# Performance work log

Measured on AMD Instinct MI355X. Metric: run time of the kernel, lower is better.

## Reference

```python
import jax, jax.numpy as jnp
import numpy as np

VOXEL_DIM = (64, 64, 64)
VOXEL_SIZE = 0.04
STRIDE = 4.0  # backbone2d_stride


def setup_inputs() -> dict:
    key = jax.random.key(0)
    k1, k2 = jax.random.split(key, 2)
    bs, nv, cin, h, w = 4, 12, 384, 64, 64
    cout = 32
    vit_feats = jax.random.normal(k1, (bs, nv, cin, h, w), dtype=jnp.float32)
    w_reduce = jax.random.normal(k2, (cout, cin), dtype=jnp.float32) * 0.05
    b_reduce = jnp.zeros((cout,), dtype=jnp.float32)
    # Realistic pinhole projections: K @ [I | t], camera ~3m from grid center.
    rng = np.random.default_rng(0)
    f, cx, cy = 128.0, 128.0, 128.0
    K = np.array([[f, 0.0, cx], [0.0, f, cy], [0.0, 0.0, 1.0]])
    projs = np.zeros((bs, nv, 3, 4), dtype=np.float32)
    for v in range(nv):
        t = np.array([0.2 * rng.standard_normal(), 0.2 * rng.standard_normal(),
                      3.0 + 0.3 * rng.standard_normal()])
        E = np.concatenate([np.eye(3), t[:, None]], axis=1)  # 3x4
        projs[:, v] = (K @ E).astype(np.float32)
    return {"vit_feats": vit_feats, "w_reduce": w_reduce,
            "b_reduce": b_reduce, "projection": jnp.asarray(projs)}


def _backproject(proj, feats):
    """proj: (b,3,4), feats: (b,c,h,w) -> volume (b,c,N), valid (b,N)."""
    nx, ny, nz = VOXEL_DIM
    N = nx * ny * nz
    b, c, h, w = feats.shape
    X, Y, Z = jnp.meshgrid(jnp.arange(nx), jnp.arange(ny), jnp.arange(nz), indexing='ij')
    coords = jnp.stack([X.ravel(), Y.ravel(), Z.ravel()]).astype(feats.dtype)  # (3, N)
    origin = jnp.array([[-nx * VOXEL_SIZE / 2],
                        [-ny * VOXEL_SIZE / 2],
                        [-nz * VOXEL_SIZE / 2]], dtype=feats.dtype)
    world = coords * VOXEL_SIZE + origin                    # (3, N)
    world = jnp.concatenate([world, jnp.ones((1, N), feats.dtype)], axis=0)  # (4, N)
    cam = jnp.einsum('bij,jn->bin', proj, world)            # (b, 3, N)
    px = jnp.round(cam[:, 0] / cam[:, 2]).astype(jnp.int32)
    py = jnp.round(cam[:, 1] / cam[:, 2]).astype(jnp.int32)
    pz = cam[:, 2]
    valid = (px >= 0) & (py >= 0) & (px < w) & (py < h) & (pz > 0)  # (b, N)
    pxc = jnp.clip(px, 0, w - 1)
    pyc = jnp.clip(py, 0, h - 1)
    # per-batch gather: feats[b, :, py, px]
    gath = jax.vmap(lambda f, yy, xx: f[:, yy, xx])(feats, pyc, pxc)  # (b, c, N)
    vol = jnp.where(valid[:, None, :], gath, jnp.zeros((), feats.dtype))
    return vol, valid


def reference(vit_feats, w_reduce, b_reduce, projection):
    bs, nv, cin, h, w = vit_feats.shape
    cout = w_reduce.shape[0]
    nx, ny, nz = VOXEL_DIM
    N = nx * ny * nz
    # 1x1 conv channel reduction
    feats = jnp.einsum('bnchw,oc->bnohw', vit_feats, w_reduce) \
            + b_reduce[None, None, :, None, None]
    # divide intrinsics rows by the 2D backbone stride
    proj = projection.at[:, :, :2, :].set(projection[:, :, :2, :] / STRIDE)
    feats_v = jnp.moveaxis(feats, 1, 0)   # (nv, b, c, h, w)
    proj_v = jnp.moveaxis(proj, 1, 0)     # (nv, b, 3, 4)

    def step(carry, xs):
        vol, cnt = carry
        p, f = xs
        v, m = _backproject(p, f)
        return (vol + v, cnt + m.astype(vol.dtype)), None

    vol0 = jnp.zeros((bs, cout, N), jnp.float32)
    cnt0 = jnp.zeros((bs, N), jnp.float32)
    (vol, cnt), _ = jax.lax.scan(step, (vol0, cnt0), (proj_v, feats_v))
    # volume / valid, zeroed where never observed
    cnt_b = cnt[:, None, :]
    out = jnp.where(cnt_b > 0, vol / jnp.maximum(cnt_b, 1.0), jnp.zeros((), vol.dtype))
    return out.reshape(bs, cout, nx, ny, nz)
```

## Files before the change

kernel.cpp:

```cpp
#include <hip/hip_runtime.h>

#define NV 12
#define CIN 384
#define COUT 32
#define HW 4096
#define NVOX 262144
#define KSTEPS 12
#define KSTEP 32
#define KPAD 33
#define PIXB 128
#define ZROW_U4 786432

typedef __attribute__((ext_vector_type(8))) short short8v;
typedef __attribute__((ext_vector_type(4))) short short4v;
typedef __attribute__((ext_vector_type(4))) float f32x4;

__device__ __forceinline__ short bf16b(float x) {
    union { float f; unsigned u; } c; c.f = x;
    unsigned r = (c.u + 0x7fffu + ((c.u >> 16) & 1u)) >> 16;
    return (short)r;
}

__global__ __launch_bounds__(256) void w_prep_kernel(
    const float* __restrict__ w, short* __restrict__ wfrag,
    short* __restrict__ feats)
{
    const int t = blockIdx.x * 256 + threadIdx.x;
    if (t < 48 * 32) {
        const int sg = t >> 5, o = t & 31;
        const int s = sg >> 2, g = sg & 3;
        short8v v;
#pragma unroll
        for (int i = 0; i < 8; ++i)
            v[i] = bf16b(w[o * CIN + s * 32 + g * 8 + i]);
        *reinterpret_cast<short8v*>(wfrag + t * 8) = v;
    } else if (t >= 1536 && t < 1540) {
        reinterpret_cast<uint4*>(feats)[ZROW_U4 + (t - 1536)] =
            make_uint4(0u, 0u, 0u, 0u);
    }
}

__global__ __launch_bounds__(256) void mv_reduce_mfma_kernel(
    const float* __restrict__ vit, const short* __restrict__ wfrag,
    const float* __restrict__ bias, short* __restrict__ feats)
{
    __shared__ float lds[PIXB][KPAD];

    const int bid  = blockIdx.x;
    const int bv   = bid >> 5;
    const int pix0 = (bid & 31) * PIXB;

    const int tid  = threadIdx.x;
    const int wave = tid >> 6;
    const int l    = tid & 63;
    const int col  = l & 15;
    const int g    = l >> 4;

    const int kk  = tid >> 4;
    const int px4 = (tid & 15) * 4;

    const float* vbase = vit + (size_t)bv * CIN * HW + pix0;
    const short8v* wf  = reinterpret_cast<const short8v*>(wfrag);

    f32x4 acc00 = {0.f, 0.f, 0.f, 0.f};
    f32x4 acc01 = {0.f, 0.f, 0.f, 0.f};
    f32x4 acc10 = {0.f, 0.f, 0.f, 0.f};
    f32x4 acc11 = {0.f, 0.f, 0.f, 0.f};

#pragma unroll
    for (int s = 0; s < KSTEPS; ++s) {
        const float* r0base = vbase + (size_t)(s * KSTEP + kk) * HW;
        const float* r1base = vbase + (size_t)(s * KSTEP + kk + 16) * HW;
        const float4 r00 = *reinterpret_cast<const float4*>(r0base + px4);
        const float4 r01 = *reinterpret_cast<const float4*>(r0base + px4 + 64);
        const float4 r10 = *reinterpret_cast<const float4*>(r1base + px4);
        const float4 r11 = *reinterpret_cast<const float4*>(r1base + px4 + 64);

        __syncthreads();
        lds[px4 + 0][kk] = r00.x;  lds[px4 + 1][kk] = r00.y;
        lds[px4 + 2][kk] = r00.z;  lds[px4 + 3][kk] = r00.w;
        lds[px4 + 64][kk] = r01.x; lds[px4 + 65][kk] = r01.y;
        lds[px4 + 66][kk] = r01.z; lds[px4 + 67][kk] = r01.w;
        lds[px4 + 0][kk + 16] = r10.x;  lds[px4 + 1][kk + 16] = r10.y;
        lds[px4 + 2][kk + 16] = r10.z;  lds[px4 + 3][kk + 16] = r10.w;
        lds[px4 + 64][kk + 16] = r11.x; lds[px4 + 65][kk + 16] = r11.y;
        lds[px4 + 66][kk + 16] = r11.z; lds[px4 + 67][kk + 16] = r11.w;
        __syncthreads();

        const float4 f0a = *reinterpret_cast<const float4*>(&lds[wave * 32 + col][8 * g]);
        const float4 f0b = *reinterpret_cast<const float4*>(&lds[wave * 32 + col][8 * g + 4]);
        const float4 f1a = *reinterpret_cast<const float4*>(&lds[wave * 32 + 16 + col][8 * g]);
        const float4 f1b = *reinterpret_cast<const float4*>(&lds[wave * 32 + 16 + col][8 * g + 4]);

        short8v bfr0, bfr1;
        bfr0[0] = bf16b(f0a.x); bfr0[1] = bf16b(f0a.y);
        bfr0[2] = bf16b(f0a.z); bfr0[3] = bf16b(f0a.w);
        bfr0[4] = bf16b(f0b.x); bfr0[5] = bf16b(f0b.y);
        bfr0[6] = bf16b(f0b.z); bfr0[7] = bf16b(f0b.w);
        bfr1[0] = bf16b(f1a.x); bfr1[1] = bf16b(f1a.y);
        bfr1[2] = bf16b(f1a.z); bfr1[3] = bf16b(f1a.w);
        bfr1[4] = bf16b(f1b.x); bfr1[5] = bf16b(f1b.y);
        bfr1[6] = bf16b(f1b.z); bfr1[7] = bf16b(f1b.w);

        const short8v a0 = wf[(s * 4 + g) * 32 + col];
        const short8v a1 = wf[(s * 4 + g) * 32 + 16 + col];

        acc00 = __builtin_amdgcn_mfma_f32_16x16x32_bf16(a0, bfr0, acc00, 0, 0, 0);
        acc01 = __builtin_amdgcn_mfma_f32_16x16x32_bf16(a1, bfr0, acc01, 0, 0, 0);
        acc10 = __builtin_amdgcn_mfma_f32_16x16x32_bf16(a0, bfr1, acc10, 0, 0, 0);
        acc11 = __builtin_amdgcn_mfma_f32_16x16x32_bf16(a1, bfr1, acc11, 0, 0, 0);
    }

    const float4 b0 = *reinterpret_cast<const float4*>(bias + 4 * g);
    const float4 b1 = *reinterpret_cast<const float4*>(bias + 16 + 4 * g);
    short* dst0 = feats + ((size_t)bv * HW + pix0 + wave * 32 + col) * COUT;
    short* dst1 = dst0 + 16 * COUT;
    short4v o00, o01, o10, o11;
    o00[0] = bf16b(acc00[0] + b0.x); o00[1] = bf16b(acc00[1] + b0.y);
    o00[2] = bf16b(acc00[2] + b0.z); o00[3] = bf16b(acc00[3] + b0.w);
    o01[0] = bf16b(acc01[0] + b1.x); o01[1] = bf16b(acc01[1] + b1.y);
    o01[2] = bf16b(acc01[2] + b1.z); o01[3] = bf16b(acc01[3] + b1.w);
    o10[0] = bf16b(acc10[0] + b0.x); o10[1] = bf16b(acc10[1] + b0.y);
    o10[2] = bf16b(acc10[2] + b0.z); o10[3] = bf16b(acc10[3] + b0.w);
    o11[0] = bf16b(acc11[0] + b1.x); o11[1] = bf16b(acc11[1] + b1.y);
    o11[2] = bf16b(acc11[2] + b1.z); o11[3] = bf16b(acc11[3] + b1.w);
    *reinterpret_cast<short4v*>(dst0 + 4 * g) = o00;
    *reinterpret_cast<short4v*>(dst0 + 16 + 4 * g) = o01;
    *reinterpret_cast<short4v*>(dst1 + 4 * g) = o10;
    *reinterpret_cast<short4v*>(dst1 + 16 + 4 * g) = o11;
}

__global__ __launch_bounds__(256) void mv_fuse_kernel(
    const unsigned short* __restrict__ feats, const float* __restrict__ proj,
    float* __restrict__ out)
{
    __shared__ double P[NV][12];

    const int tid = threadIdx.x;
    const unsigned gid = blockIdx.x * 256u + tid;
    const unsigned vox = gid >> 2;
    const int r = tid & 3;
    const int lane = tid & 63;
    const int b = vox >> 18;
    const int n = vox & (NVOX - 1);

    if (tid < NV * 12) {
        const int v = tid / 12, e = tid - v * 12;
        const int row = e >> 2;
        const float s = (row < 2) ? 0.25f : 1.0f;
        P[v][e] = (double)(proj[((b * NV + v) * 3 + row) * 4 + (e & 3)] * s);
    }
    __syncthreads();

    const int k = n & 63, j = (n >> 6) & 63, i = n >> 12;
    const double wx = (double)i * 0.04 - 1.28;
    const double wy = (double)j * 0.04 - 1.28;
    const double wz = (double)k * 0.04 - 1.28;

    int off[3];
    int cnt = 0;
    const int bbase = b * (NV * HW * 4);
#pragma unroll
    for (int s = 0; s < 3; ++s) {
        const double* p = P[4 * s + r];
        const double cz = p[8] * wx + p[9] * wy + p[10] * wz + p[11];
        const double cx = p[0] * wx + p[1] * wy + p[2] * wz + p[3];
        const double cy = p[4] * wx + p[5] * wy + p[6] * wz + p[7];
        const double u = rint(cx / cz);
        const double t = rint(cy / cz);
        const bool valid = (cz > 0.0) & (u >= 0.0) & (u <= 63.0) &
                           (t >= 0.0) & (t <= 63.0);
        const double uc = fmin(fmax(u, 0.0), 63.0);
        const double tc = fmin(fmax(t, 0.0), 63.0);
        const int pix = (int)uc + 64 * (int)tc;
        off[s] = valid ? (bbase + ((4 * s + r) * HW + pix) * 4) : ZROW_U4;
        cnt += valid ? 1 : 0;
    }
    cnt += __shfl_xor(cnt, 1);
    cnt += __shfl_xor(cnt, 2);

    float acc[8];
#pragma unroll
    for (int q = 0; q < 8; ++q) acc[q] = 0.0f;

    const uint4* f4 = reinterpret_cast<const uint4*>(feats);
#pragma unroll
    for (int v = 0; v < NV; ++v) {
        const int src = (lane & ~3) | (v & 3);
        const int ov = __shfl(off[v >> 2], src, 64);
        const uint4 u4 = f4[ov + r];
        acc[0] += __uint_as_float(u4.x << 16);
        acc[1] += __uint_as_float(u4.x & 0xffff0000u);
        acc[2] += __uint_as_float(u4.y << 16);
        acc[3] += __uint_as_float(u4.y & 0xffff0000u);
        acc[4] += __uint_as_float(u4.z << 16);
        acc[5] += __uint_as_float(u4.z & 0xffff0000u);
        acc[6] += __uint_as_float(u4.w << 16);
        acc[7] += __uint_as_float(u4.w & 0xffff0000u);
    }

    const float sc = (cnt > 0) ? (1.0f / (float)cnt) : 0.0f;
    float* ob = out + (size_t)b * COUT * NVOX + (size_t)(8 * r) * NVOX + n;
#pragma unroll
    for (int q = 0; q < 8; ++q)
        ob[(size_t)q * NVOX] = acc[q] * sc;
}

extern "C" void kernel_launch(void* const* d_in, const int* in_sizes, int n_in,
                              void* d_out, int out_size, void* d_ws, size_t ws_size,
                              hipStream_t stream) {
    const float* vit  = (const float*)d_in[0];
    const float* w    = (const float*)d_in[1];
    const float* bias = (const float*)d_in[2];
    const float* proj = (const float*)d_in[3];
    float* out = (float*)d_out;

    short* wfrag = (short*)d_ws;
    short* feats = (short*)((char*)d_ws + 48 * 32 * 8 * 2);

    w_prep_kernel<<<7, 256, 0, stream>>>(w, wfrag, feats);

    mv_reduce_mfma_kernel<<<1536, 256, 0, stream>>>(vit, wfrag, bias, feats);

    mv_fuse_kernel<<<16384, 256, 0, stream>>>(
        (const unsigned short*)feats, proj, out);
}
```

Before: 131.4 us.

## Stream vit tiles into LDS with global_load_lds and prefetch next k-step

The channel-reduction GEMM now loads input tiles straight from global memory into LDS using global_load_lds, in a [k][pixel] layout with a per-wave rotated source index to avoid bank conflicts. The next k-step is prefetched into LDS after the current fragments are read into registers, so loads overlap the bf16 conversion and MFMA work. This removes the register staging and scalar transposed LDS stores. Separately, the backprojection replaces two double divides with one reciprocal and two multiplies. That can change rounding for pixels that sit exactly on a rint boundary.

```diff
diff --git a/kernel.cpp b/kernel.cpp
--- a/kernel.cpp
+++ b/kernel.cpp
@@ -7,7 +7,6 @@
 #define NVOX 262144
 #define KSTEPS 12
 #define KSTEP 32
-#define KPAD 33
 #define PIXB 128
 #define ZROW_U4 786432
 
@@ -19,6 +18,12 @@
     union { float f; unsigned u; } c; c.f = x;
     unsigned r = (c.u + 0x7fffu + ((c.u >> 16) & 1u)) >> 16;
     return (short)r;
+}
+
+__device__ __forceinline__ void load_lds16(const float* g, float* l) {
+    __builtin_amdgcn_global_load_lds(
+        (const __attribute__((address_space(1))) void*)g,
+        (__attribute__((address_space(3))) void*)l, 16, 0, 0);
 }
 
 __global__ __launch_bounds__(256) void w_prep_kernel(
@@ -44,7 +49,7 @@
     const float* __restrict__ vit, const short* __restrict__ wfrag,
     const float* __restrict__ bias, short* __restrict__ feats)
 {
-    __shared__ float lds[PIXB][KPAD];
+    __shared__ float lds[KSTEP][PIXB];
 
     const int bid  = blockIdx.x;
     const int bv   = bid >> 5;
@@ -55,12 +60,15 @@
     const int l    = tid & 63;
     const int col  = l & 15;
     const int g    = l >> 4;
-
-    const int kk  = tid >> 4;
-    const int px4 = (tid & 15) * 4;
+    const int lhalf = l >> 5;
+    const int lq    = l & 31;
+    const int srcq  = (lq - 2 * wave) & 31;
 
     const float* vbase = vit + (size_t)bv * CIN * HW + pix0;
     const short8v* wf  = reinterpret_cast<const short8v*>(wfrag);
+
+    const int rc0 = (wave * 32 + col + 8 * g) & 127;
+    const int rc1 = (wave * 32 + col + 16 + 8 * g) & 127;
 
     f32x4 acc00 = {0.f, 0.f, 0.f, 0.f};
     f32x4 acc01 = {0.f, 0.f, 0.f, 0.f};
@@ -68,39 +76,39 @@
     f32x4 acc11 = {0.f, 0.f, 0.f, 0.f};
 
 #pragma unroll
+    for (int i = 0; i < 4; ++i) {
+        const int row = 8 * wave + 2 * i;
+        load_lds16(vbase + (size_t)(row + lhalf) * HW + srcq * 4, &lds[row][0]);
+    }
+
+#pragma unroll
     for (int s = 0; s < KSTEPS; ++s) {
-        const float* r0base = vbase + (size_t)(s * KSTEP + kk) * HW;
-        const float* r1base = vbase + (size_t)(s * KSTEP + kk + 16) * HW;
-        const float4 r00 = *reinterpret_cast<const float4*>(r0base + px4);
-        const float4 r01 = *reinterpret_cast<const float4*>(r0base + px4 + 64);
-        const float4 r10 = *reinterpret_cast<const float4*>(r1base + px4);
-        const float4 r11 = *reinterpret_cast<const float4*>(r1base + px4 + 64);
-
         __syncthreads();
-        lds[px4 + 0][kk] = r00.x;  lds[px4 + 1][kk] = r00.y;
-        lds[px4 + 2][kk] = r00.z;  lds[px4 + 3][kk] = r00.w;
-        lds[px4 + 64][kk] = r01.x; lds[px4 + 65][kk] = r01.y;
-        lds[px4 + 66][kk] = r01.z; lds[px4 + 67][kk] = r01.w;
-        lds[px4 + 0][kk + 16] = r10.x;  lds[px4 + 1][kk + 16] = r10.y;
-        lds[px4 + 2][kk + 16] = r10.z;  lds[px4 + 3][kk + 16] = r10.w;
-        lds[px4 + 64][kk + 16] = r11.x; lds[px4 + 65][kk + 16] = r11.y;
-        lds[px4 + 66][kk + 16] = r11.z; lds[px4 + 67][kk + 16] = r11.w;
+
+        float fr0[8], fr1[8];
+#pragma unroll
+        for (int i = 0; i < 8; ++i) {
+            fr0[i] = lds[8 * g + i][rc0];
+            fr1[i] = lds[8 * g + i][rc1];
+        }
         __syncthreads();
 
-        const float4 f0a = *reinterpret_cast<const float4*>(&lds[wave * 32 + col][8 * g]);
-        const float4 f0b = *reinterpret_cast<const float4*>(&lds[wave * 32 + col][8 * g + 4]);
-        const float4 f1a = *reinterpret_cast<const float4*>(&lds[wave * 32 + 16 + col][8 * g]);
-        const float4 f1b = *reinterpret_cast<const float4*>(&lds[wave * 32 + 16 + col][8 * g + 4]);
+        if (s + 1 < KSTEPS) {
+#pragma unroll
+            for (int i = 0; i < 4; ++i) {
+                const int row = 8 * wave + 2 * i;
+                load_lds16(vbase + (size_t)((s + 1) * KSTEP + row + lhalf) * HW
+                               + srcq * 4,
+                           &lds[row][0]);
+            }
+        }
 
         short8v bfr0, bfr1;
-        bfr0[0] = bf16b(f0a.x); bfr0[1] = bf16b(f0a.y);
-        bfr0[2] = bf16b(f0a.z); bfr0[3] = bf16b(f0a.w);
-        bfr0[4] = bf16b(f0b.x); bfr0[5] = bf16b(f0b.y);
-        bfr0[6] = bf16b(f0b.z); bfr0[7] = bf16b(f0b.w);
-        bfr1[0] = bf16b(f1a.x); bfr1[1] = bf16b(f1a.y);
-        bfr1[2] = bf16b(f1a.z); bfr1[3] = bf16b(f1a.w);
-        bfr1[4] = bf16b(f1b.x); bfr1[5] = bf16b(f1b.y);
-        bfr1[6] = bf16b(f1b.z); bfr1[7] = bf16b(f1b.w);
+#pragma unroll
+        for (int i = 0; i < 8; ++i) {
+            bfr0[i] = bf16b(fr0[i]);
+            bfr1[i] = bf16b(fr1[i]);
+        }
 
         const short8v a0 = wf[(s * 4 + g) * 32 + col];
         const short8v a1 = wf[(s * 4 + g) * 32 + 16 + col];
@@ -166,8 +174,9 @@
         const double cz = p[8] * wx + p[9] * wy + p[10] * wz + p[11];
         const double cx = p[0] * wx + p[1] * wy + p[2] * wz + p[3];
         const double cy = p[4] * wx + p[5] * wy + p[6] * wz + p[7];
-        const double u = rint(cx / cz);
-        const double t = rint(cy / cz);
+        const double rcz = 1.0 / cz;
+        const double u = rint(cx * rcz);
+        const double t = rint(cy * rcz);
         const bool valid = (cz > 0.0) & (u >= 0.0) & (u <= 63.0) &
                            (t >= 0.0) & (t <= 63.0);
         const double uc = fmin(fmax(u, 0.0), 63.0);
```

Measured after the change: 125.6 us. 4.4% less time.
